# Optimization experiments

Hardware: AMD Instinct MI355X
Metric: run time of the kernel (lower is better)

The kernel has to match this reference:

```python
import jax, jax.numpy as jnp
import numpy as np

L, D, H, N, R = 4, 256, 512, 16, 8  # layers, d_model, hidden=2*d_model, state_dim, dt_rank
OUT_LEN, IN_DIM = 96, 32
EPS = 1e-5


def _layernorm(v, g, b):
    m = jnp.mean(v, axis=-1, keepdims=True)
    var = jnp.mean((v - m) ** 2, axis=-1, keepdims=True)
    return (v - m) / jnp.sqrt(var + EPS) * g + b


def _pos_encoding(T, d):
    pos = jnp.arange(T, dtype=jnp.float32)[:, None]
    div = jnp.exp(jnp.arange(0, d, 2, dtype=jnp.float32) * (-np.log(10000.0) / d))
    pe = jnp.zeros((T, d), dtype=jnp.float32)
    pe = pe.at[:, 0::2].set(jnp.sin(pos * div))
    pe = pe.at[:, 1::2].set(jnp.cos(pos * div))
    return pe


def setup_inputs() -> dict:
    key = jax.random.key(0)
    ks = jax.random.split(key, 20)
    inp = {
        "x": jax.random.normal(ks[0], (8, 1024, IN_DIM), dtype=jnp.float32),
        "emb_w": jax.random.normal(ks[1], (D, IN_DIM), dtype=jnp.float32) * 0.1,
        "emb_b": jnp.zeros((D,), dtype=jnp.float32),
        "norm_g": jnp.ones((L, D), dtype=jnp.float32),
        "norm_b": jnp.zeros((L, D), dtype=jnp.float32),
        "in_w": jax.random.normal(ks[2], (L, H, D), dtype=jnp.float32) * (1.0 / np.sqrt(D)),
        "conv_w": jax.random.normal(ks[3], (L, H, 1, 3), dtype=jnp.float32) * 0.5,
        "A_p": jax.random.normal(ks[4], (L, H, N), dtype=jnp.float32) * 0.01,
        "D_p": jnp.ones((L, H), dtype=jnp.float32),
        "dt1_w": jax.random.normal(ks[5], (L, R, H), dtype=jnp.float32) * (1.0 / np.sqrt(H)),
        "dt1_b": jnp.zeros((L, R), dtype=jnp.float32),
        "dt2_w": jax.random.normal(ks[6], (L, H, R), dtype=jnp.float32) * (1.0 / np.sqrt(R)),
        "dt2_b": jnp.zeros((L, H), dtype=jnp.float32),
        "out_w": jax.random.normal(ks[7], (L, D, H), dtype=jnp.float32) * (1.0 / np.sqrt(H)),
        "final_g": jnp.ones((D,), dtype=jnp.float32),
        "final_b": jnp.zeros((D,), dtype=jnp.float32),
        "head1_w": jax.random.normal(ks[8], (D, D), dtype=jnp.float32) * (1.0 / np.sqrt(D)),
        "head1_b": jnp.zeros((D,), dtype=jnp.float32),
        "head2_w": jax.random.normal(ks[9], (OUT_LEN, D), dtype=jnp.float32) * (1.0 / np.sqrt(D)),
        "head2_b": jnp.zeros((OUT_LEN,), dtype=jnp.float32),
    }
    return inp


def _mamba_block(h, g, b, in_w, conv_w, A_p, D_p, dt1_w, dt1_b, dt2_w, dt2_b, out_w):
    res = h
    v = _layernorm(h, g, b)            # [B,T,D]
    v = jnp.einsum('btd,hd->bth', v, in_w)  # [B,T,H]
    # depthwise conv1d, kernel 3, padding 1, groups=H
    vc = jnp.transpose(v, (0, 2, 1))   # [B,H,T]
    vc = jax.lax.conv_general_dilated(vc, conv_w, window_strides=(1,),
                                      padding=[(1, 1)], feature_group_count=H,
                                      dimension_numbers=('NCH', 'OIH', 'NCH'))
    v = jnp.transpose(jax.nn.silu(vc), (0, 2, 1))  # [B,T,H]
    dt = jax.nn.relu(jnp.einsum('bth,rh->btr', v, dt1_w) + dt1_b)
    dt = jnp.einsum('btr,hr->bth', dt, dt2_w) + dt2_b
    dt = jax.nn.softplus(dt)           # [B,T,H]
    A = -jnp.exp(A_p)                  # [H,N]
    safe_A = jnp.where(jnp.abs(A) < 1e-5, jnp.ones_like(A), A)

    B_sz = v.shape[0]
    state0 = jnp.zeros((B_sz, H, N), dtype=v.dtype)

    def step(state, inp):
        x_t, dt_t = inp  # [B,H] each
        dA = A * dt_t[..., None]            # [B,H,N]
        discA = jnp.exp(dA)
        discB = (discA - 1.0) / safe_A * dt_t[..., None]
        state = discA * state + discB * x_t[..., None]
        y = jnp.einsum('bhn,hn->bh', state, A_p) + D_p * x_t
        return state, y

    xs = (jnp.transpose(v, (1, 0, 2)), jnp.transpose(dt, (1, 0, 2)))  # [T,B,H]
    _, ys = jax.lax.scan(step, state0, xs)
    y = jnp.transpose(ys, (1, 0, 2))   # [B,T,H]
    return res + jnp.einsum('bth,dh->btd', y, out_w)


def reference(x, emb_w, emb_b, norm_g, norm_b, in_w, conv_w, A_p, D_p,
              dt1_w, dt1_b, dt2_w, dt2_b, out_w, final_g, final_b,
              head1_w, head1_b, head2_w, head2_b):
    h = jnp.einsum('bti,di->btd', x, emb_w) + emb_b  # [B,T,D]
    h = h + _pos_encoding(h.shape[1], D)[None]
    for l in range(L):
        h = _mamba_block(h, norm_g[l], norm_b[l], in_w[l], conv_w[l], A_p[l],
                         D_p[l], dt1_w[l], dt1_b[l], dt2_w[l], dt2_b[l], out_w[l])
    h = _layernorm(h, final_g, final_b)
    h = h[:, -1, :]                    # last token [B,D]
    h = jax.nn.silu(h @ head1_w.T + head1_b)
    return h @ head2_w.T + head2_b     # [B, OUT_LEN]
```

## Files before the change

kernel.cpp:

```cpp
#include <hip/hip_runtime.h>
#include <hip/hip_bf16.h>
#include <math.h>

#define BB 8
#define TT 1024
#define DD 256
#define HH 512
#define NN 16
#define RR 8
#define OUT_LEN 96
#define IN_DIM 32
#define MM (BB*TT)

#define SC 16
#define CC (TT/SC)

typedef unsigned short u16;
typedef unsigned int u32;
typedef __attribute__((ext_vector_type(8))) short short8;
typedef __attribute__((ext_vector_type(8))) unsigned short u16x8;
typedef __attribute__((ext_vector_type(4))) float float4v;

__device__ __forceinline__ u16 f2bf(float f) {
    __hip_bfloat16 h = __float2bfloat16(f);
    return *(u16*)&h;
}
__device__ __forceinline__ float bf2f(u16 u) {
    u32 v = ((u32)u) << 16;
    return *(float*)&v;
}

#define GLD_LDS16(src, dst) __builtin_amdgcn_global_load_lds( \
    (const __attribute__((address_space(1))) void*)(src),     \
    (__attribute__((address_space(3))) void*)(dst), 16, 0, 0)

__global__ __launch_bounds__(256) void embed_ln_cvt_kernel(
    const float* __restrict__ x, const float* __restrict__ emb_w,
    const float* __restrict__ emb_b,
    const float* __restrict__ g, const float* __restrict__ b,
    float* __restrict__ h, u16* __restrict__ lnout,
    const float* __restrict__ w_in, u16* __restrict__ wbf_in,
    const float* __restrict__ w_out, u16* __restrict__ wbf_out, int nw)
{
    int bid = blockIdx.x;
    if (bid >= MM) {
        int i = (bid - MM) * 256 + threadIdx.x;
        if (i < nw) wbf_in[i] = f2bf(w_in[i]);
        else        wbf_out[i - nw] = f2bf(w_out[i - nw]);
        return;
    }

    int bt = bid;
    int d  = threadIdx.x;
    int t  = bt & (TT - 1);

    __shared__ float xs[IN_DIM];
    __shared__ float red[4], red2[4];
    if (threadIdx.x < IN_DIM) xs[threadIdx.x] = x[bt * IN_DIM + threadIdx.x];
    __syncthreads();

    const float* w = emb_w + d * IN_DIM;
    float acc = emb_b[d];
#pragma unroll
    for (int i = 0; i < IN_DIM; i++) acc = fmaf(xs[i], w[i], acc);

    int i2 = d & ~1;
    float div = expf(-(float)i2 * (logf(10000.0f) / (float)DD));
    float arg = (float)t * div;
    float pe = (d & 1) ? cosf(arg) : sinf(arg);
    float val = acc + pe;
    h[bt * DD + d] = val;

    float s = val;
#pragma unroll
    for (int o = 32; o > 0; o >>= 1) s += __shfl_down(s, o);
    int lane = d & 63, wave = d >> 6;
    if (lane == 0) red[wave] = s;
    __syncthreads();
    float mean = (red[0] + red[1] + red[2] + red[3]) * (1.0f / DD);

    float c = val - mean;
    float s2 = c * c;
#pragma unroll
    for (int o = 32; o > 0; o >>= 1) s2 += __shfl_down(s2, o);
    if (lane == 0) red2[wave] = s2;
    __syncthreads();
    float var = (red2[0] + red2[1] + red2[2] + red2[3]) * (1.0f / DD);

    lnout[bt * DD + d] = f2bf(c * rsqrtf(var + 1e-5f) * g[d] + b[d]);
}

template<int BM, int BN, int OUT_BF16>
__global__ __launch_bounds__(256) void gemm_bf16(
    const u16* __restrict__ A, const u16* __restrict__ B,
    void* __restrict__ Cv, int M, int N, int K, int addC)
{
    constexpr int BK = 64;
    constexpr int MT = BM / 32;
    constexpr int NT = BN / 32;
    static_assert(BN == 64, "B staging assumes BN==64");

    __shared__ __align__(16) u16 Al[8][BM][8];
    __shared__ __align__(16) u16 Bl[8][BN][8];

    const int tid = threadIdx.x;
    const int bm = blockIdx.y * BM;
    const int bn = blockIdx.x * BN;
    const int wid = tid >> 6, lane = tid & 63;
    const int wm = wid >> 1, wn = wid & 1;
    const int lq = lane >> 4, lm = lane & 15;

    float4v acc[MT][NT];
#pragma unroll
    for (int i = 0; i < MT; i++)
#pragma unroll
        for (int j = 0; j < NT; j++) acc[i][j] = (float4v){0.f, 0.f, 0.f, 0.f};

    for (int k0 = 0; k0 < K; k0 += BK) {
#pragma unroll
        for (int it = 0; it < (8 * BM) / 256; it++) {
            int c = it * 256 + tid;
            int q = c / BM, row = c % BM;
            GLD_LDS16(A + (size_t)(bm + row) * K + k0 + q * 8, &Al[q][row][0]);
        }
#pragma unroll
        for (int it = 0; it < (8 * BN) / 256; it++) {
            int c = it * 256 + tid;
            int q = c / BN, row = c % BN;
            GLD_LDS16(B + (size_t)(bn + row) * K + k0 + q * 8, &Bl[q][row][0]);
        }
        __syncthreads();

        short8 af[2][MT], bf[2][NT];
#pragma unroll
        for (int kk = 0; kk < 2; kk++) {
#pragma unroll
            for (int mt = 0; mt < MT; mt++)
                af[kk][mt] = *(const short8*)&Al[kk * 4 + lq][wm * (BM / 2) + mt * 16 + lm][0];
#pragma unroll
            for (int nt = 0; nt < NT; nt++)
                bf[kk][nt] = *(const short8*)&Bl[kk * 4 + lq][wn * (BN / 2) + nt * 16 + lm][0];
        }

#pragma unroll
        for (int kk = 0; kk < 2; kk++)
#pragma unroll
            for (int mt = 0; mt < MT; mt++)
#pragma unroll
                for (int nt = 0; nt < NT; nt++)
                    acc[mt][nt] = __builtin_amdgcn_mfma_f32_16x16x32_bf16(
                        af[kk][mt], bf[kk][nt], acc[mt][nt], 0, 0, 0);
        __syncthreads();
    }

#pragma unroll
    for (int mt = 0; mt < MT; mt++)
#pragma unroll
        for (int nt = 0; nt < NT; nt++) {
            int row0 = bm + wm * (BM / 2) + mt * 16 + lq * 4;
            int col  = bn + wn * (BN / 2) + nt * 16 + lm;
#pragma unroll
            for (int r = 0; r < 4; r++) {
                float vv = acc[mt][nt][r];
                if (OUT_BF16) {
                    ((u16*)Cv)[(size_t)(row0 + r) * N + col] = f2bf(vv);
                } else {
                    float* cp = (float*)Cv + (size_t)(row0 + r) * N + col;
                    if (addC) vv += *cp;
                    *cp = vv;
                }
            }
        }
}

__global__ __launch_bounds__(256) void gemm2_ln(
    const u16* __restrict__ A, const u16* __restrict__ B,
    float* __restrict__ h,
    const float* __restrict__ g, const float* __restrict__ bb,
    u16* __restrict__ lnout, int doLN)
{
    constexpr int BM = 32;
    __shared__ __align__(16) u16 Al[8][BM][8];
    __shared__ __align__(16) u16 Bl[8][256][8];
    __shared__ float rs[2][BM], qs[2][BM];

    const int tid = threadIdx.x;
    const int bm = blockIdx.x * BM;
    const int wid = tid >> 6, lane = tid & 63;
    const int wm = wid >> 1, wn = wid & 1;
    const int lq = lane >> 4, lm = lane & 15;

    float4v acc[8];
#pragma unroll
    for (int j = 0; j < 8; j++) acc[j] = (float4v){0.f, 0.f, 0.f, 0.f};

    for (int k0 = 0; k0 < 512; k0 += 64) {
        {
            int q = tid >> 5, row = tid & 31;
            GLD_LDS16(A + (size_t)(bm + row) * 512 + k0 + q * 8, &Al[q][row][0]);
        }
#pragma unroll
        for (int it = 0; it < 8; it++) {
            int c = it * 256 + tid;
            int q = c >> 8, row = c & 255;
            GLD_LDS16(B + (size_t)row * 512 + k0 + q * 8, &Bl[q][row][0]);
        }
        __syncthreads();

        short8 af[2], bf[2][8];
#pragma unroll
        for (int kk = 0; kk < 2; kk++) {
            af[kk] = *(const short8*)&Al[kk * 4 + lq][wm * 16 + lm][0];
#pragma unroll
            for (int nt = 0; nt < 8; nt++)
                bf[kk][nt] = *(const short8*)&Bl[kk * 4 + lq][wn * 128 + nt * 16 + lm][0];
        }
#pragma unroll
        for (int kk = 0; kk < 2; kk++)
#pragma unroll
            for (int nt = 0; nt < 8; nt++)
                acc[nt] = __builtin_amdgcn_mfma_f32_16x16x32_bf16(
                    af[kk], bf[kk][nt], acc[nt], 0, 0, 0);
        __syncthreads();
    }

    float val[4][8];
    float s1[4] = {0.f, 0.f, 0.f, 0.f}, s2[4] = {0.f, 0.f, 0.f, 0.f};
#pragma unroll
    for (int r = 0; r < 4; r++) {
        int row = bm + wm * 16 + lq * 4 + r;
#pragma unroll
        for (int nt = 0; nt < 8; nt++) {
            int col = wn * 128 + nt * 16 + lm;
            float v = acc[nt][r] + h[(size_t)row * DD + col];
            val[r][nt] = v;
            s1[r] += v;
            s2[r] = fmaf(v, v, s2[r]);
            h[(size_t)row * DD + col] = v;
        }
    }
#pragma unroll
    for (int r = 0; r < 4; r++) {
#pragma unroll
        for (int o = 1; o < 16; o <<= 1) {
            s1[r] += __shfl_xor(s1[r], o);
            s2[r] += __shfl_xor(s2[r], o);
        }
    }
    if (lm == 0) {
#pragma unroll
        for (int r = 0; r < 4; r++) {
            rs[wn][wm * 16 + lq * 4 + r] = s1[r];
            qs[wn][wm * 16 + lq * 4 + r] = s2[r];
        }
    }
    __syncthreads();

    if (doLN) {
#pragma unroll
        for (int r = 0; r < 4; r++) {
            int i = wm * 16 + lq * 4 + r;
            int row = bm + i;
            float mean = (rs[0][i] + rs[1][i]) * (1.0f / DD);
            float var  = (qs[0][i] + qs[1][i]) * (1.0f / DD) - mean * mean;
            float rstd = rsqrtf(var + 1e-5f);
#pragma unroll
            for (int nt = 0; nt < 8; nt++) {
                int col = wn * 128 + nt * 16 + lm;
                lnout[(size_t)row * DD + col] =
                    f2bf((val[r][nt] - mean) * rstd * g[col] + bb[col]);
            }
        }
    }
}

__global__ __launch_bounds__(256) void conv_dt1_kernel(
    const u16* __restrict__ v, const float* __restrict__ cwg,
    const float* __restrict__ w1g, const float* __restrict__ b1g,
    u16* __restrict__ vsb, float* __restrict__ dtr)
{
    __shared__ float w1s[RR * 2 * 256];
    int tid = threadIdx.x;
    {
        int lane = tid & 63, rc = tid >> 6;
#pragma unroll
        for (int i = 0; i < 4; i++) {
            int rci = rc + i * 4;
            int r = rci >> 1, jc = rci & 1;
            float4 wv = *(const float4*)(w1g + r * HH + lane * 8 + jc * 4);
            *(float4*)&w1s[rci * 256 + lane * 4] = wv;
        }
    }
    __syncthreads();

    int wave = tid >> 6, lane = tid & 63;
    int m = blockIdx.x * 4 + wave;
    int t = m & (TT - 1);
    int h0 = lane * 8;

    const u16* vrow = v + (size_t)m * HH + h0;
    u16x8 x0 = *(const u16x8*)vrow;
    u16x8 xm = (t > 0)      ? *(const u16x8*)(vrow - HH) : (u16x8)(0);
    u16x8 xp = (t < TT - 1) ? *(const u16x8*)(vrow + HH) : (u16x8)(0);

    const float* wp = cwg + h0 * 3;
    float a[8];
    u16x8 o;
#pragma unroll
    for (int j = 0; j < 8; j++) {
        float s = wp[j * 3] * bf2f(xm[j]);
        s = fmaf(wp[j * 3 + 1], bf2f(x0[j]), s);
        s = fmaf(wp[j * 3 + 2], bf2f(xp[j]), s);
        s = s / (1.0f + __expf(-s));
        a[j] = s;
        o[j] = f2bf(s);
    }
    *(u16x8*)(vsb + (size_t)m * HH + h0) = o;

    float acc[RR];
#pragma unroll
    for (int r = 0; r < RR; r++) {
        float4 wlo = *(const float4*)&w1s[(r * 2 + 0) * 256 + lane * 4];
        float4 whi = *(const float4*)&w1s[(r * 2 + 1) * 256 + lane * 4];
        float s = a[0] * wlo.x;
        s = fmaf(a[1], wlo.y, s);
        s = fmaf(a[2], wlo.z, s);
        s = fmaf(a[3], wlo.w, s);
        s = fmaf(a[4], whi.x, s);
        s = fmaf(a[5], whi.y, s);
        s = fmaf(a[6], whi.z, s);
        s = fmaf(a[7], whi.w, s);
        acc[r] = s;
    }
#pragma unroll
    for (int r = 0; r < RR; r++) {
#pragma unroll
        for (int o2 = 1; o2 < 64; o2 <<= 1) acc[r] += __shfl_xor(acc[r], o2);
    }
    if (lane == 0) {
#pragma unroll
        for (int r = 0; r < RR; r++) acc[r] = fmaxf(acc[r] + b1g[r], 0.0f);
        *(float4*)(dtr + (size_t)m * RR)     = make_float4(acc[0], acc[1], acc[2], acc[3]);
        *(float4*)(dtr + (size_t)m * RR + 4) = make_float4(acc[4], acc[5], acc[6], acc[7]);
    }
}

__device__ __forceinline__ float softplus_f(float s) {
    return (s > 20.0f) ? s : __logf(1.0f + __expf(s));
}

__global__ __launch_bounds__(256, 4) void scan_pass1(
    const u16* __restrict__ vs, const float* __restrict__ dtr,
    const float* __restrict__ dt2_w, const float* __restrict__ dt2_b,
    const float* __restrict__ A_p,
    u16* __restrict__ Lst, float* __restrict__ sdt)
{
    int h = blockIdx.x * 256 + threadIdx.x;
    int c = blockIdx.y;
    int b = blockIdx.z;

    __shared__ float ds[SC * RR];
    {
        const float* drow = dtr + ((size_t)b * TT + (size_t)c * SC) * RR;
        if (threadIdx.x < SC * RR) ds[threadIdx.x] = drow[threadIdx.x];
    }

    float A2[NN], invA[NN], st[NN];
    const float* ap = A_p + h * NN;
#pragma unroll
    for (int n = 0; n < NN; n++) {
        float a = -__expf(ap[n]);
        A2[n] = a * 1.44269504f;
        invA[n] = 1.0f / a;
        st[n] = 0.0f;
    }
    float w2[RR];
#pragma unroll
    for (int r = 0; r < RR; r++) w2[r] = dt2_w[h * RR + r];
    float b2 = dt2_b[h];

    const u16* vbase = vs + ((size_t)b * TT + (size_t)c * SC) * HH + h;
    float xv = bf2f(vbase[0]);
    __syncthreads();

    float s_dt = 0.0f;
#pragma unroll 2
    for (int t = 0; t < SC; t++) {
        float xn = (t + 1 < SC) ? bf2f(vbase[(size_t)(t + 1) * HH]) : 0.0f;
        float s = b2;
#pragma unroll
        for (int r = 0; r < RR; r++) s = fmaf(ds[t * RR + r], w2[r], s);
        float dt = softplus_f(s);
        s_dt += dt;
        float dtx = dt * xv;
#pragma unroll
        for (int n = 0; n < NN; n++) {
            float e = __builtin_amdgcn_exp2f(A2[n] * dt);
            float u = invA[n] * dtx;
            st[n] = fmaf(e, st[n] + u, -u);
        }
        xv = xn;
    }

    size_t base = (((size_t)c * BB + b) * HH + h) * NN;
    u16x8 lo, hi;
#pragma unroll
    for (int n = 0; n < 8; n++) { lo[n] = f2bf(st[n]); hi[n] = f2bf(st[n + 8]); }
    *(u16x8*)(Lst + base)     = lo;
    *(u16x8*)(Lst + base + 8) = hi;
    sdt[((size_t)c * BB + b) * HH + h] = s_dt;
}

__global__ __launch_bounds__(256) void scan_carry(
    const float* __restrict__ A_p, const float* __restrict__ sdt,
    u16* __restrict__ Lst)
{
    int i = blockIdx.x * 256 + threadIdx.x;
    int n  = i & (NN - 1);
    int bh = i >> 4;
    int h  = bh & (HH - 1);
    int b  = bh >> 9;

    float A = -__expf(A_p[h * NN + n]);
    float E = 0.0f;
    size_t sidx = (size_t)b * HH + h;
    const size_t stride = (size_t)BB * HH;
    float sd = sdt[sidx];
    u16 Lu = Lst[sidx * NN + n];
    for (int c = 0; c < CC; c++) {
        float nsd = 0.0f; u16 nLu = 0;
        if (c + 1 < CC) {
            size_t nidx = sidx + stride;
            nsd = sdt[nidx];
            nLu = Lst[nidx * NN + n];
        }
        float P = __expf(A * sd);
        float Lc = bf2f(Lu);
        Lst[sidx * NN + n] = f2bf(E);
        E = fmaf(P, E, Lc);
        sidx += stride; sd = nsd; Lu = nLu;
    }
}

__global__ __launch_bounds__(256, 4) void scan_pass2(
    const u16* __restrict__ vs,
    const float* __restrict__ dtr,
    const float* __restrict__ dt2_w,
    const float* __restrict__ dt2_b,
    const float* __restrict__ A_p, const float* __restrict__ D_p,
    const u16* __restrict__ carry,
    u16* __restrict__ y)
{
    int h = blockIdx.x * 256 + threadIdx.x;
    int c = blockIdx.y;
    int b = blockIdx.z;

    __shared__ float ds[SC * RR];
    {
        const float* drow = dtr + ((size_t)b * TT + (size_t)c * SC) * RR;
        if (threadIdx.x < SC * RR) ds[threadIdx.x] = drow[threadIdx.x];
    }

    float A2[NN], invA[NN], Ap[NN], st[NN];
    const float* app = A_p + h * NN;
    size_t cbase = (((size_t)c * BB + b) * HH + h) * NN;
    {
        u16x8 lo = *(const u16x8*)(carry + cbase);
        u16x8 hi = *(const u16x8*)(carry + cbase + 8);
#pragma unroll
        for (int n = 0; n < 8; n++) { st[n] = bf2f(lo[n]); st[n + 8] = bf2f(hi[n]); }
    }
#pragma unroll
    for (int n = 0; n < NN; n++) {
        float apv = app[n];
        Ap[n] = apv;
        float a = -__expf(apv);
        A2[n] = a * 1.44269504f;
        invA[n] = 1.0f / a;
    }
    float w2[RR];
#pragma unroll
    for (int r = 0; r < RR; r++) w2[r] = dt2_w[h * RR + r];
    float b2 = dt2_b[h];
    float Dp = D_p[h];

    const u16* vbase = vs + ((size_t)b * TT + (size_t)c * SC) * HH + h;
    u16*       ybase = y  + ((size_t)b * TT + (size_t)c * SC) * HH + h;
    float xv = bf2f(vbase[0]);
    __syncthreads();

#pragma unroll 2
    for (int t = 0; t < SC; t++) {
        float xn = (t + 1 < SC) ? bf2f(vbase[(size_t)(t + 1) * HH]) : 0.0f;
        float s = b2;
#pragma unroll
        for (int r = 0; r < RR; r++) s = fmaf(ds[t * RR + r], w2[r], s);
        float dt = softplus_f(s);
        float dtx = dt * xv;
        float acc = Dp * xv;
#pragma unroll
        for (int n = 0; n < NN; n++) {
            float e = __builtin_amdgcn_exp2f(A2[n] * dt);
            float u = invA[n] * dtx;
            st[n] = fmaf(e, st[n] + u, -u);
            acc = fmaf(st[n], Ap[n], acc);
        }
        ybase[(size_t)t * HH] = f2bf(acc);
        xv = xn;
    }
}

__global__ __launch_bounds__(256) void head_kernel(
    const float* __restrict__ h,
    const float* __restrict__ fg, const float* __restrict__ fb,
    const float* __restrict__ w1, const float* __restrict__ b1,
    const float* __restrict__ w2, const float* __restrict__ b2,
    float* __restrict__ out)
{
    int b = blockIdx.x;
    int d = threadIdx.x;
    __shared__ float hn[DD], s1[DD];
    __shared__ float red[4];

    float v = h[((size_t)b * TT + (TT - 1)) * DD + d];

    float s = v;
#pragma unroll
    for (int o = 32; o > 0; o >>= 1) s += __shfl_down(s, o);
    int lane = d & 63, wave = d >> 6;
    if (lane == 0) red[wave] = s;
    __syncthreads();
    float mean = (red[0] + red[1] + red[2] + red[3]) * (1.0f / DD);
    __syncthreads();

    float c = v - mean;
    float s2 = c * c;
#pragma unroll
    for (int o = 32; o > 0; o >>= 1) s2 += __shfl_down(s2, o);
    if (lane == 0) red[wave] = s2;
    __syncthreads();
    float var = (red[0] + red[1] + red[2] + red[3]) * (1.0f / DD);

    hn[d] = c * rsqrtf(var + 1e-5f) * fg[d] + fb[d];
    __syncthreads();

    float a1 = b1[d];
    const float* w1r = w1 + d * DD;
#pragma unroll 8
    for (int k = 0; k < DD; k++) a1 = fmaf(hn[k], w1r[k], a1);
    s1[d] = a1 / (1.0f + __expf(-a1));
    __syncthreads();

    if (d < OUT_LEN) {
        float a2 = b2[d];
        const float* w2r = w2 + d * DD;
#pragma unroll 8
        for (int k = 0; k < DD; k++) a2 = fmaf(s1[k], w2r[k], a2);
        out[b * OUT_LEN + d] = a2;
    }
}

extern "C" void kernel_launch(void* const* d_in, const int* in_sizes, int n_in,
                              void* d_out, int out_size, void* d_ws, size_t ws_size,
                              hipStream_t stream)
{
    (void)in_sizes; (void)n_in; (void)out_size; (void)ws_size;

    const float* x       = (const float*)d_in[0];
    const float* emb_w   = (const float*)d_in[1];
    const float* emb_b   = (const float*)d_in[2];
    const float* norm_g  = (const float*)d_in[3];
    const float* norm_b  = (const float*)d_in[4];
    const float* in_w    = (const float*)d_in[5];
    const float* conv_w  = (const float*)d_in[6];
    const float* A_p     = (const float*)d_in[7];
    const float* D_p     = (const float*)d_in[8];
    const float* dt1_w   = (const float*)d_in[9];
    const float* dt1_b   = (const float*)d_in[10];
    const float* dt2_w   = (const float*)d_in[11];
    const float* dt2_b   = (const float*)d_in[12];
    const float* out_w   = (const float*)d_in[13];
    const float* final_g = (const float*)d_in[14];
    const float* final_b = (const float*)d_in[15];
    const float* head1_w = (const float*)d_in[16];
    const float* head1_b = (const float*)d_in[17];
    const float* head2_w = (const float*)d_in[18];
    const float* head2_b = (const float*)d_in[19];
    float* outp = (float*)d_out;

    char* ws = (char*)d_ws;
    float* h     = (float*)ws;                ws += (size_t)MM * DD * 4;
    u16*   vbf   = (u16*)ws;                  ws += (size_t)MM * HH * 2;
    u16*   vsb   = (u16*)ws;                  ws += (size_t)MM * HH * 2;
    u16*   ybf   = (u16*)ws;                  ws += (size_t)MM * HH * 2;
    u16*   lnbuf = (u16*)ws;                  ws += (size_t)MM * DD * 2;
    float* dtr   = (float*)ws;                ws += (size_t)MM * RR * 4;
    u16*   Lst   = (u16*)ws;                  ws += (size_t)CC * BB * HH * NN * 2;
    float* sdt   = (float*)ws;                ws += (size_t)CC * BB * HH * 4;
    u16*   wbf_in  = (u16*)ws;                ws += (size_t)4 * HH * DD * 2;
    u16*   wbf_out = (u16*)ws;                ws += (size_t)4 * DD * HH * 2;

    const int NW = 4 * HH * DD;
    embed_ln_cvt_kernel<<<MM + (2 * NW) / 256, 256, 0, stream>>>(
        x, emb_w, emb_b, norm_g, norm_b, h, lnbuf,
        in_w, wbf_in, out_w, wbf_out, NW);

    for (int l = 0; l < 4; l++) {
        gemm_bf16<128, 64, 1><<<dim3(HH / 64, MM / 128), 256, 0, stream>>>(
            lnbuf, wbf_in + (size_t)l * HH * DD, vbf, MM, HH, DD, 0);
        conv_dt1_kernel<<<MM / 4, 256, 0, stream>>>(
            vbf, conv_w + (size_t)l * HH * 3,
            dt1_w + (size_t)l * RR * HH, dt1_b + l * RR, vsb, dtr);

        scan_pass1<<<dim3(HH / 256, CC, BB), 256, 0, stream>>>(
            vsb, dtr, dt2_w + (size_t)l * HH * RR, dt2_b + l * HH,
            A_p + (size_t)l * HH * NN, Lst, sdt);
        scan_carry<<<(BB * HH * NN) / 256, 256, 0, stream>>>(
            A_p + (size_t)l * HH * NN, sdt, Lst);
        scan_pass2<<<dim3(HH / 256, CC, BB), 256, 0, stream>>>(
            vsb, dtr, dt2_w + (size_t)l * HH * RR, dt2_b + l * HH,
            A_p + (size_t)l * HH * NN, D_p + l * HH, Lst, ybf);

        const float* g_next = (l < 3) ? (norm_g + (l + 1) * DD) : final_g;
        const float* b_next = (l < 3) ? (norm_b + (l + 1) * DD) : final_b;
        gemm2_ln<<<MM / 32, 256, 0, stream>>>(
            ybf, wbf_out + (size_t)l * DD * HH, h, g_next, b_next,
            lnbuf, (l < 3) ? 1 : 0);
    }

    head_kernel<<<BB, 256, 0, stream>>>(h, final_g, final_b,
                                        head1_w, head1_b, head2_w, head2_b, outp);
}
```

Baseline: 486.0 us.

## Parallelize chunk carry with warp scan, swizzle GEMM blocks, use fast trig

The chunk-carry recurrence, which walked 64 chunks serially per (b,h,n) thread, becomes a wavefront-level Hillis-Steele scan: one wave per (b,h), one lane per chunk, with each lane loading and storing its 16-state vector in vectorized form. This removes a long serial dependency chain and its strided scalar memory traffic. The GEMM remaps block indices into groups of 8 row-tiles to improve L2 reuse of the shared operand. The positional-encoding embedding switches to fast __expf, __sinf and __cosf intrinsics with a precomputed constant, which may lose some accuracy at large arguments.

Measured after the change: 499.4 us. +2.8%, slower.

```diff
diff --git a/kernel.cpp b/kernel.cpp
--- a/kernel.cpp
+++ b/kernel.cpp
@@ -65,9 +65,9 @@
     for (int i = 0; i < IN_DIM; i++) acc = fmaf(xs[i], w[i], acc);
 
     int i2 = d & ~1;
-    float div = expf(-(float)i2 * (logf(10000.0f) / (float)DD));
+    float div = __expf(-(float)i2 * 0.0359778918f);
     float arg = (float)t * div;
-    float pe = (d & 1) ? cosf(arg) : sinf(arg);
+    float pe = (d & 1) ? __cosf(arg) : __sinf(arg);
     float val = acc + pe;
     h[bt * DD + d] = val;
 
@@ -104,8 +104,13 @@
     __shared__ __align__(16) u16 Bl[8][BN][8];
 
     const int tid = threadIdx.x;
-    const int bm = blockIdx.y * BM;
-    const int bn = blockIdx.x * BN;
+    const int nbx = gridDim.x;
+    const int o   = blockIdx.x + nbx * blockIdx.y;
+    const int r8  = o & 7, q8 = o >> 3;
+    const int bxs = q8 % nbx;
+    const int bys = (q8 / nbx) * 8 + r8;
+    const int bm = bys * BM;
+    const int bn = bxs * BN;
     const int wid = tid >> 6, lane = tid & 63;
     const int wm = wid >> 1, wn = wid & 1;
     const int lq = lane >> 4, lm = lane & 15;
@@ -411,35 +416,38 @@
     sdt[((size_t)c * BB + b) * HH + h] = s_dt;
 }
 
-__global__ __launch_bounds__(256) void scan_carry(
+__global__ __launch_bounds__(256) void scan_carry_par(
     const float* __restrict__ A_p, const float* __restrict__ sdt,
     u16* __restrict__ Lst)
 {
-    int i = blockIdx.x * 256 + threadIdx.x;
-    int n  = i & (NN - 1);
-    int bh = i >> 4;
-    int h  = bh & (HH - 1);
-    int b  = bh >> 9;
-
-    float A = -__expf(A_p[h * NN + n]);
-    float E = 0.0f;
-    size_t sidx = (size_t)b * HH + h;
-    const size_t stride = (size_t)BB * HH;
+    int gw   = (blockIdx.x << 2) | (threadIdx.x >> 6);
+    int lane = threadIdx.x & 63;
+    int b = gw >> 9;
+    int h = gw & 511;
+
+    size_t sidx = ((size_t)lane * BB + b) * HH + h;
     float sd = sdt[sidx];
-    u16 Lu = Lst[sidx * NN + n];
-    for (int c = 0; c < CC; c++) {
-        float nsd = 0.0f; u16 nLu = 0;
-        if (c + 1 < CC) {
-            size_t nidx = sidx + stride;
-            nsd = sdt[nidx];
-            nLu = Lst[nidx * NN + n];
-        }
-        float P = __expf(A * sd);
-        float Lc = bf2f(Lu);
-        Lst[sidx * NN + n] = f2bf(E);
-        E = fmaf(P, E, Lc);
-        sidx += stride; sd = nsd; Lu = nLu;
-    }
+    const float* ap = A_p + h * NN;
+    u16x8 Llo = *(const u16x8*)(Lst + sidx * NN);
+    u16x8 Lhi = *(const u16x8*)(Lst + sidx * NN + 8);
+    u16x8 Elo, Ehi;
+#pragma unroll
+    for (int n = 0; n < NN; n++) {
+        float An = -__expf(ap[n]);
+        float p  = __expf(An * sd);
+        float lv = bf2f((n < 8) ? Llo[n] : Lhi[n - 8]);
+#pragma unroll
+        for (int d2 = 1; d2 < 64; d2 <<= 1) {
+            float pp = __shfl_up(p, d2);
+            float pl = __shfl_up(lv, d2);
+            if (lane >= d2) { lv = fmaf(pl, p, lv); p = pp * p; }
+        }
+        float E = __shfl_up(lv, 1);
+        if (lane == 0) E = 0.0f;
+        if (n < 8) Elo[n] = f2bf(E); else Ehi[n - 8] = f2bf(E);
+    }
+    *(u16x8*)(Lst + sidx * NN)     = Elo;
+    *(u16x8*)(Lst + sidx * NN + 8) = Ehi;
 }
 
 __global__ __launch_bounds__(256, 4) void scan_pass2(
@@ -615,7 +623,7 @@
         scan_pass1<<<dim3(HH / 256, CC, BB), 256, 0, stream>>>(
             vsb, dtr, dt2_w + (size_t)l * HH * RR, dt2_b + l * HH,
             A_p + (size_t)l * HH * NN, Lst, sdt);
-        scan_carry<<<(BB * HH * NN) / 256, 256, 0, stream>>>(
+        scan_carry_par<<<(BB * HH) / 4, 256, 0, stream>>>(
             A_p + (size_t)l * HH * NN, sdt, Lst);
         scan_pass2<<<dim3(HH / 256, CC, BB), 256, 0, stream>>>(
             vsb, dtr, dt2_w + (size_t)l * HH * RR, dt2_b + l * HH,
```
